# Kernel tuning notes

Hardware: AMD Instinct MI355X
Metric: run time of the kernel (lower is better)

Reference implementation:

```python
import jax, jax.numpy as jnp
import numpy as np
from jax import lax

N_SIN = 3

def _bn(x, g, b, m, v, eps):
    sh = [1] * x.ndim; sh[1] = -1
    r = lambda t: t.reshape(sh)
    return (x - r(m)) / jnp.sqrt(r(v) + eps) * r(g) + r(b)

def _conv2d(x, w, b, padding):
    y = lax.conv_general_dilated(x, w, (1, 1), padding,
                                 dimension_numbers=('NCHW', 'OIHW', 'NCHW'))
    return y + b[None, :, None, None]

def _causal_conv1d(x, w, b):
    k = w.shape[-1]
    y = lax.conv_general_dilated(x, w, (1,), [(k - 1, 0)],
                                 dimension_numbers=('NCH', 'OIH', 'NCH'))
    return y + b[None, :, None]

def _se(x, w1, w2):
    y = x.mean(axis=2)                                   # [B,C] global avg pool
    y = jax.nn.sigmoid(jax.nn.relu(y @ w1.T) @ w2.T)
    return x * y[:, :, None]

def _kan(x, W1, W2, B1, B2):
    # x: [B,din]; per-edge tiny MLP: sin/cos embed -> linear -> silu -> linear
    omega = (2.0 ** jnp.arange(N_SIN)).astype(x.dtype)   # [n_sin]
    ox = x[..., None] * omega                            # [B,din,n_sin]
    feat = jnp.concatenate([x[..., None], jnp.sin(ox), jnp.cos(ox)], axis=-1)  # [B,din,7]
    h = jnp.einsum('bif,ijhf->bijh', feat, W1) + B1[None]  # [B,din,dout,h]
    h = jax.nn.silu(h)
    out = jnp.einsum('bijh,ijh->bij', h, W2[:, :, 0, :]) + B2[None, :, :, 0]
    return out.sum(axis=1)                               # [B,dout]

def _lstm(x, w_ih, w_hh, b_ih, b_hh):
    B, T, E = x.shape
    H = w_hh.shape[1]
    def step(carry, xt):
        h, c = carry
        g = xt @ w_ih.T + h @ w_hh.T + (b_ih + b_hh)
        i, f, gg, o = jnp.split(g, 4, axis=-1)           # torch gate order i,f,g,o
        c = jax.nn.sigmoid(f) * c + jax.nn.sigmoid(i) * jnp.tanh(gg)
        h = jax.nn.sigmoid(o) * jnp.tanh(c)
        return (h, c), h
    init = (jnp.zeros((B, H), x.dtype), jnp.zeros((B, H), x.dtype))
    _, hs = lax.scan(step, init, jnp.swapaxes(x, 0, 1))
    return jnp.swapaxes(hs, 0, 1)                        # [B,T,H]

def _cluster(hidden):
    B, T, H = hidden.shape
    last = hidden[:, -1, :]
    hn = hidden / jnp.maximum(jnp.linalg.norm(hidden, axis=-1, keepdims=True), 1e-8)
    sim = jnp.einsum('bth,bsh->bts', hn, hn)
    sim = jnp.exp(-5.5 * (1.0 - sim))
    sim = sim * (1.0 - jnp.eye(T, dtype=sim.dtype))      # zero diagonal
    # 2-D prefix sums replace the O(T) python loop over block means
    S = jnp.cumsum(jnp.cumsum(sim, axis=1), axis=2)
    Sii = jnp.diagonal(S, axis1=1, axis2=2)[:, :T - 1]   # sum of [:i,:i]
    R = S[:, -1, :T - 1]                                 # sum of [:, :i]
    C = S[:, :T - 1, -1]                                 # sum of [:i, :]
    tot = S[:, -1, -1][:, None]
    i_f = jnp.arange(1, T, dtype=sim.dtype)
    dist = (Sii / i_f**2
            + (tot - R - C + Sii) / (T - i_f)**2
            - (C - Sii) / (i_f * (T - i_f))
            - (R - Sii) / (i_f * (T - i_f)))             # [B,T-1]
    cuts = jnp.argmax(dist, axis=1) + 1                  # [B]
    mask = (jnp.arange(T)[None, :] < cuts[:, None]).astype(hidden.dtype)
    corr = (hidden * mask[:, :, None]).sum(axis=1) / cuts[:, None].astype(hidden.dtype)
    return last, corr

def reference(x, we1, be1, bn_e1_g, bn_e1_b, bn_e1_m, bn_e1_v, we2, be2, bn_e2_g, bn_e2_b, bn_e2_m, bn_e2_v, w_ih, w_hh, b_ih, b_hh, mu_W1, mu_W2, mu_B1, mu_B2, std_W1, std_W2, std_B1, std_B2, muc_W1, muc_W2, muc_B1, muc_B2, stdc_W1, stdc_W2, stdc_B1, stdc_B2, fc_W1, fc_W2, fc_B1, fc_B2, wc1, bc1, bn1_g, bn1_b, bn1_m, bn1_v, se1_w1, se1_w2, wc2, bc2, bn2_g, bn2_b, bn2_m, bn2_v, se2_w1, se2_w2, wc3, bc3, bn3_g, bn3_b, bn3_m, bn3_v, eps1, eps2):
    gelu = lambda t: jax.nn.gelu(t, approximate=False)
    x = jnp.transpose(x, (0, 2, 1))                      # shuffle: [B,T,F]->[B,F,T]
    h2d = _conv2d(x[:, None], we1, be1, 'SAME')          # [B,4E,F,T]
    h2d = gelu(_bn(h2d, bn_e1_g, bn_e1_b, bn_e1_m, bn_e1_v, 1e-5))
    h2d = _conv2d(h2d, we2, be2, 'VALID')                # [B,E,1,T]
    h2d = gelu(_bn(h2d, bn_e2_g, bn_e2_b, bn_e2_m, bn_e2_v, 1e-5))
    x_src = jnp.transpose(h2d[:, :, 0, :], (0, 2, 1))    # [B,T,E]
    hseq = _lstm(x_src, w_ih, w_hh, b_ih, b_hh)          # [B,T,H]
    out, corr = _cluster(hseq)
    mu = _kan(corr, mu_W1, mu_W2, mu_B1, mu_B2)
    std = jax.nn.softplus(_kan(corr, std_W1, std_W2, std_B1, std_B2) - 5.0)
    z = mu + std * eps1
    x_z = jnp.concatenate([out, z], axis=1)              # [B,2H]
    mu_c = _kan(x_z, muc_W1, muc_W2, muc_B1, muc_B2)
    std_c = jax.nn.softplus(_kan(x_z, stdc_W1, stdc_W2, stdc_B1, stdc_B2) - 5.0)
    x1 = mu_c + std_c * eps2                             # dropout = identity (eval)
    x2 = jnp.transpose(x, (0, 2, 1))                     # [B,T,F]: channels = seq_len
    x2 = gelu(_bn(_causal_conv1d(x2, wc1, bc1), bn1_g, bn1_b, bn1_m, bn1_v, 1e-3))
    x2 = _se(x2, se1_w1, se1_w2)
    x2 = gelu(_bn(_causal_conv1d(x2, wc2, bc2), bn2_g, bn2_b, bn2_m, bn2_v, 1e-3))
    x2 = _se(x2, se2_w1, se2_w2)
    x2 = gelu(_bn(_causal_conv1d(x2, wc3, bc3), bn3_g, bn3_b, bn3_m, bn3_v, 1e-3))
    x2 = x2.mean(axis=2)                                 # [B,conv3_nf]
    x_all = jnp.concatenate([x1, x2], axis=1)            # [B, H+conv3_nf]
    return _kan(x_all, fc_W1, fc_W2, fc_B1, fc_B2)       # [B,num_classes]

def setup_inputs():
    key = jax.random.key(0)
    ks = iter(jax.random.split(key, 128))
    f32 = jnp.float32
    def n(shape, s=0.05):
        return s * jax.random.normal(next(ks), shape, f32)
    def bn_params(c):
        g = 1.0 + 0.05 * jax.random.normal(next(ks), (c,), f32)
        b = 0.05 * jax.random.normal(next(ks), (c,), f32)
        m = 0.05 * jax.random.normal(next(ks), (c,), f32)
        v = jax.random.uniform(next(ks), (c,), f32, 0.5, 1.5)
        return g, b, m, v
    def kan_params(din, dout, h=32, feat=1 + 2 * N_SIN):
        s = (2.0 / (feat + h)) ** 0.5
        return (n((din, dout, h, feat), s), n((din, dout, 1, h), s),
                jnp.zeros((din, dout, h), f32), jnp.zeros((din, dout, 1), f32))
    B, T, F_, E, H = 32, 256, 32, 64, 128
    inp = {}
    inp['x'] = jax.random.normal(next(ks), (B, T, F_), f32)
    inp['we1'] = n((4 * E, 1, 1, 8)); inp['be1'] = n((4 * E,))
    inp['bn_e1_g'], inp['bn_e1_b'], inp['bn_e1_m'], inp['bn_e1_v'] = bn_params(4 * E)
    inp['we2'] = n((E, 4 * E, F_, 1)); inp['be2'] = n((E,))
    inp['bn_e2_g'], inp['bn_e2_b'], inp['bn_e2_m'], inp['bn_e2_v'] = bn_params(E)
    inp['w_ih'] = n((4 * H, E)); inp['w_hh'] = n((4 * H, H))
    inp['b_ih'] = n((4 * H,)); inp['b_hh'] = n((4 * H,))
    for nm, (di, do) in [('mu', (H, H)), ('std', (H, H)), ('muc', (2 * H, H)), ('stdc', (2 * H, H)), ('fc', (2 * H, 10))]:
        w1, w2, b1, b2 = kan_params(di, do)
        inp[nm + '_W1'], inp[nm + '_W2'], inp[nm + '_B1'], inp[nm + '_B2'] = w1, w2, b1, b2
    inp['wc1'] = n((128, T, 8)); inp['bc1'] = n((128,))
    inp['bn1_g'], inp['bn1_b'], inp['bn1_m'], inp['bn1_v'] = bn_params(128)
    inp['se1_w1'] = n((8, 128)); inp['se1_w2'] = n((128, 8))
    inp['wc2'] = n((256, 128, 5)); inp['bc2'] = n((256,))
    inp['bn2_g'], inp['bn2_b'], inp['bn2_m'], inp['bn2_v'] = bn_params(256)
    inp['se2_w1'] = n((16, 256)); inp['se2_w2'] = n((256, 16))
    inp['wc3'] = n((128, 256, 3)); inp['bc3'] = n((128,))
    inp['bn3_g'], inp['bn3_b'], inp['bn3_m'], inp['bn3_v'] = bn_params(128)
    inp['eps1'] = jax.random.normal(next(ks), (B, H), f32)
    inp['eps2'] = jax.random.normal(next(ks), (B, H), f32)
    return inp
```

## Files before the change

### kernel.cpp

```cpp
#include <hip/hip_runtime.h>
#include <hip/hip_bf16.h>
#include <math.h>

typedef __hip_bfloat16 bf16;

#define DEV static __device__ __forceinline__

DEV float geluf(float x){ return 0.5f*x*(1.0f + erff(x*0.70710678118654752f)); }
DEV float sigmf(float x){ return 1.0f/(1.0f + __expf(-x)); }
DEV float softplusf(float x){ return (x > 15.f) ? x : log1pf(__expf(x)); }
DEV float tanhfast(float x){ float e = __expf(2.f*x); return fmaf(-2.f, 1.f/(e+1.f), 1.f); }

typedef __attribute__((ext_vector_type(8))) short v8s;
typedef __attribute__((ext_vector_type(4))) float v4f;
typedef _Float16 f16;
typedef f16 h2 __attribute__((ext_vector_type(2)));
typedef f16 f16x8 __attribute__((ext_vector_type(8)));
typedef unsigned u32x4 __attribute__((ext_vector_type(4)));

DEV float dot2f(h2 a, h2 b, float c){
#if __has_builtin(__builtin_amdgcn_fdot2)
  return __builtin_amdgcn_fdot2(a, b, c, false);
#else
  return fmaf((float)a.y, (float)b.y, fmaf((float)a.x, (float)b.x, c));
#endif
}

DEV h2 geth2(f16x8 v, int j){ h2 r; r.x = v[2*j]; r.y = v[2*j+1]; return r; }

DEV void lds_barrier(){
  asm volatile("s_waitcnt lgkmcnt(0)" ::: "memory");
  __builtin_amdgcn_s_barrier();
  __builtin_amdgcn_sched_barrier(0);
}

enum : size_t {
  OFF_W1F   = 0,
  OFF_B1F   = 2048,
  OFF_S2E   = 2304,
  OFF_B2E   = 2368,
  OFF_WIHT  = 2432,
  OFF_BIASG = 35200,
  OFF_WHHT  = 35712,
  OFF_EPI1S = 101248,
  OFF_EPI1B = 101376,
  OFF_EPI2S = 101504,
  OFF_EPI2B = 101760,
  OFF_EPI3S = 102016,
  OFF_EPI3B = 102144,
  OFF_WE2B  = 102272,
  OFF_XSRC  = 364416,
  OFF_GX    = 888704,
  OFF_HSEQ  = 5083008,
  OFF_HN    = 6131584,
  OFF_PCOL  = 7180160,
  OFF_CCOL  = 7188352,
  OFF_CUTS  = 7196544,
  OFF_LAST  = 7196576,
  OFF_CORR  = 7200672,
  OFF_FEATA = 7204768,
  OFF_XZ    = 7241632,
  OFF_FEATB = 7249824,
  OFF_WC3P  = 7315360,
  OFF_WC2P  = 7446432,
  OFF_KP    = 7708576,
  OFF_B2S   = 7741344,
  OFF_X2F   = 7839648,
  OFF_XALL  = 7843744,
  OFF_FEATC = 7851936,
  WS_FLOATS = 7909280
};

__global__ __launch_bounds__(256) void prep_kernel(
    const float* we1, const float* be1,
    const float* e1g, const float* e1b, const float* e1m, const float* e1v,
    const float* we2, const float* be2, const float* e2g, const float* e2b, const float* e2m, const float* e2v,
    const float* wih, const float* whh, const float* bih, const float* bhh,
    const float* bc1, const float* c1g, const float* c1b, const float* c1m, const float* c1v,
    const float* bc2, const float* c2g, const float* c2b, const float* c2m, const float* c2v,
    const float* bc3, const float* c3g, const float* c3b, const float* c3m, const float* c3v,
    const float* muB2, const float* sdB2, const float* mcB2, const float* scB2, const float* fcB2,
    const float* wc2, const float* wc3,
    float* ws)
{
  int idx = blockIdx.x*256 + threadIdx.x;
  if(idx < 2048){
    int o = idx>>3;
    float s = e1g[o] * rsqrtf(e1v[o] + 1e-5f);
    ws[OFF_W1F + idx] = we1[idx] * s;
  } else if(idx < 2304){
    int o = idx - 2048;
    float s = e1g[o] * rsqrtf(e1v[o] + 1e-5f);
    ws[OFF_B1F + o] = s*(be1[o] - e1m[o]) + e1b[o];
  } else if(idx < 2368){
    int e = idx - 2304;
    float s = e2g[e] * rsqrtf(e2v[e] + 1e-5f);
    ws[OFF_S2E + e] = s;
    ws[OFF_B2E + e] = s*(be2[e] - e2m[e]) + e2b[e];
  } else if(idx < 35136){
    int q = idx - 2368; int e = q>>9, g = q&511;
    ws[OFF_WIHT + q] = wih[g*64 + e];
  } else if(idx < 35648){
    int g = idx - 35136;
    ws[OFF_BIASG + g] = bih[g] + bhh[g];
  } else if(idx < 101184){
    int q = idx - 35648;
    if(q < 32768){
      int k2 = q>>9, g = q&511;
      h2 v;
      v.x = (f16)whh[g*128 + 2*k2];
      v.y = (f16)whh[g*128 + 2*k2 + 1];
      ((h2*)(ws + OFF_WHHT))[g*64 + k2] = v;
    }
  } else if(idx < 101312){
    int o = idx - 101184;
    float s = c1g[o] * rsqrtf(c1v[o] + 1e-3f);
    ws[OFF_EPI1S + o] = s;
    ws[OFF_EPI1B + o] = s*(bc1[o] - c1m[o]) + c1b[o];
  } else if(idx < 101568){
    int o = idx - 101312;
    float s = c2g[o] * rsqrtf(c2v[o] + 1e-3f);
    ws[OFF_EPI2S + o] = s;
    ws[OFF_EPI2B + o] = s*(bc2[o] - c2m[o]) + c2b[o];
  } else if(idx < 101696){
    int o = idx - 101568;
    float s = c3g[o] * rsqrtf(c3v[o] + 1e-3f);
    ws[OFF_EPI3S + o] = s;
    ws[OFF_EPI3B + o] = s*(bc3[o] - c3m[o]) + c3b[o];
  } else if(idx < 625984){
    int q = idx - 101696;
    int o = q >> 11, rem = q & 2047;
    int e = rem >> 5, f = rem & 31;
    bf16* Wr = (bf16*)(ws + OFF_WE2B);
    Wr[q] = __float2bfloat16(we2[(size_t)e*8192 + o*32 + f]);
  } else if(idx < 626112){
    int j = idx - 625984; float s = 0.f;
    for(int i=0;i<128;i++) s += muB2[i*128+j];
    ws[OFF_B2S + j] = s;
  } else if(idx < 626240){
    int j = idx - 626112; float s = 0.f;
    for(int i=0;i<128;i++) s += sdB2[i*128+j];
    ws[OFF_B2S + 128 + j] = s;
  } else if(idx < 626368){
    int j = idx - 626240; float s = 0.f;
    for(int i=0;i<256;i++) s += mcB2[i*128+j];
    ws[OFF_B2S + 256 + j] = s;
  } else if(idx < 626496){
    int j = idx - 626368; float s = 0.f;
    for(int i=0;i<256;i++) s += scB2[i*128+j];
    ws[OFF_B2S + 384 + j] = s;
  } else if(idx < 626506){
    int j = idx - 626496; float s = 0.f;
    for(int i=0;i<256;i++) s += fcB2[i*10+j];
    ws[OFF_B2S + 512 + j] = s;
  } else if(idx < 888650){
    int q = idx - 626506;
    int o = q >> 10, rem = q & 1023;
    int c = rem >> 3, k = rem & 7;
    ws[OFF_WC2P + q] = (k < 5) ? wc2[(size_t)o*640 + c*5 + k] : 0.f;
  } else if(idx < 1019722){
    int q = idx - 888650;
    int o = q >> 10, rem = q & 1023;
    int c = rem >> 2, k = rem & 3;
    ws[OFF_WC3P + q] = (k < 3) ? wc3[(size_t)o*768 + c*3 + k] : 0.f;
  }
}

__global__ __launch_bounds__(256,1) void encoder_kernel(
    const float* __restrict__ x, const float* __restrict__ w1f, const float* __restrict__ b1f,
    const float* __restrict__ s2e, const float* __restrict__ b2e,
    const bf16* __restrict__ Wr, float* __restrict__ x_src)
{
  __shared__ float xs[39*32];
  __shared__ float w1s[2048];
  __shared__ float b1s[256];
  __shared__ __align__(16) unsigned short At[2][32*136];
  __shared__ __align__(16) unsigned short Bt[2][4*2560];

  int blk = blockIdx.x; int b = blk>>3; int t0 = (blk&7)*32;
  int tid = threadIdx.x;

  for(int i=tid;i<2048;i+=256) w1s[i] = w1f[i];
  b1s[tid] = b1f[tid];
  for(int i=tid;i<39*32;i+=256){
    int r=i>>5, f=i&31; int t=t0-3+r;
    xs[i] = (t>=0 && t<256) ? x[(b*256+t)*32+f] : 0.f;
  }
  __syncthreads();

  int f = tid & 31, tq = tid >> 5;
  int lane = tid & 63, w = tid >> 6;
  int wm = w & 1, wn = w >> 1;
  int m0 = wm*16, n0 = wn*32;
  int l15 = lane & 15, quad = lane >> 4;

  const v8s* Wv = (const v8s*)Wr;

  auto stage = [&](int cc, int buf){
    v8s bw[4];
    #pragma unroll
    for(int i=0;i<4;i++) bw[i] = Wv[cc*1024 + i*256 + tid];
    unsigned short aval[16];
    #pragma unroll
    for(int ol=0;ol<4;ol++){
      int o = cc*4 + ol;
      float wv[8];
      #pragma unroll
      for(int j=0;j<8;j++) wv[j] = w1s[o*8+j];
      float bb = b1s[o];
      #pragma unroll
      for(int i=0;i<4;i++){
        int tl = tq*4 + i;
        float c = bb;
        #pragma unroll
        for(int j=0;j<8;j++) c = fmaf(wv[j], xs[(tl+j)*32+f], c);
        aval[ol*4+i] = ((__hip_bfloat16_raw)__float2bfloat16(geluf(c))).x;
      }
    }
    #pragma unroll
    for(int ol=0;ol<4;ol++){
      #pragma unroll
      for(int i=0;i<4;i++)
        At[buf][(tq*4+i)*136 + ol*32 + f] = aval[ol*4+i];
    }
    #pragma unroll
    for(int i=0;i<4;i++){
      int j = i*256 + tid;
      int ol = j>>8, e = (j&255)>>2, f8 = j&3;
      *(v8s*)&Bt[buf][ol*2560 + e*40 + f8*8] = bw[i];
    }
  };

  stage(0, 0);
  __syncthreads();

  v4f acc0 = {0.f,0.f,0.f,0.f}, acc1 = {0.f,0.f,0.f,0.f};

  for(int c=0;c<64;c++){
    int p = c & 1, q = p ^ 1;
    if(c < 63) stage(c+1, q);
    #pragma unroll
    for(int ol=0;ol<4;ol++){
      v8s av = *(const v8s*)&At[p][(m0+l15)*136 + ol*32 + quad*8];
      v8s b0 = *(const v8s*)&Bt[p][ol*2560 + (n0+l15)*40 + quad*8];
      v8s b1 = *(const v8s*)&Bt[p][ol*2560 + (n0+16+l15)*40 + quad*8];
      acc0 = __builtin_amdgcn_mfma_f32_16x16x32_bf16(av, b0, acc0, 0, 0, 0);
      acc1 = __builtin_amdgcn_mfma_f32_16x16x32_bf16(av, b1, acc1, 0, 0, 0);
    }
    __syncthreads();
  }

  #pragma unroll
  for(int r=0;r<4;r++){
    int t = t0 + m0 + quad*4 + r;
    int e0 = n0 + l15;
    float v0 = geluf(s2e[e0]*acc0[r] + b2e[e0]);
    x_src[((size_t)(b*256+t))*64 + e0] = v0;
    int e1 = e0 + 16;
    float v1 = geluf(s2e[e1]*acc1[r] + b2e[e1]);
    x_src[((size_t)(b*256+t))*64 + e1] = v1;
  }
}

__global__ __launch_bounds__(256) void gates_kernel(
    const float* x_src, const float* wihT, const float* biasg, float* gx)
{
  __shared__ float xsh[32*64];
  int blk = blockIdx.x; int b = blk>>3, t0 = (blk&7)*32;
  int tid = threadIdx.x;
  for(int i=tid;i<2048;i+=256) xsh[i] = x_src[((size_t)b*256+t0)*64 + i];
  __syncthreads();
  int g0 = tid, g1 = tid + 256;
  float acc0[32], acc1[32];
  #pragma unroll
  for(int tt=0;tt<32;tt++){ acc0[tt]=0.f; acc1[tt]=0.f; }
  for(int e=0;e<64;e++){
    float w0 = wihT[e*512+g0], w1 = wihT[e*512+g1];
    #pragma unroll
    for(int tt=0;tt<32;tt++){
      float xv = xsh[tt*64+e];
      acc0[tt] = fmaf(xv, w0, acc0[tt]);
      acc1[tt] = fmaf(xv, w1, acc1[tt]);
    }
  }
  float bg0 = biasg[g0], bg1 = biasg[g1];
  #pragma unroll
  for(int tt=0;tt<32;tt++){
    gx[((size_t)b*256+t0+tt)*512 + g0] = acc0[tt] + bg0;
    gx[((size_t)b*256+t0+tt)*512 + g1] = acc1[tt] + bg1;
  }
}

#define LSTM_STEP(GI, GF, GG, GO, PR, PW, T)                                 \
  {                                                                          \
    const f16x8* hp = (const f16x8*)&hsh[PR][half*64];                       \
    f16x8 hvv[8];                                                            \
    _Pragma("unroll")                                                        \
    for(int q=0;q<8;q++) hvv[q] = hp[q];                                     \
    float si=0.f, sf=0.f, sg=0.f, so=0.f;                                    \
    _Pragma("unroll")                                                        \
    for(int q=0;q<8;q++){                                                    \
      f16x8 Wi = __builtin_bit_cast(f16x8, wi[q]);                           \
      f16x8 Wf = __builtin_bit_cast(f16x8, wf[q]);                           \
      f16x8 Wg = __builtin_bit_cast(f16x8, wg[q]);                           \
      f16x8 Wo = __builtin_bit_cast(f16x8, wo[q]);                           \
      f16x8 hq = hvv[q];                                                     \
      _Pragma("unroll")                                                      \
      for(int j=0;j<4;j++){                                                  \
        h2 hj = geth2(hq, j);                                                \
        si = dot2f(hj, geth2(Wi,j), si);                                     \
        sf = dot2f(hj, geth2(Wf,j), sf);                                     \
        sg = dot2f(hj, geth2(Wg,j), sg);                                     \
        so = dot2f(hj, geth2(Wo,j), so);                                     \
      }                                                                      \
    }                                                                        \
    si += __shfl_xor(si, 32, 64);                                            \
    sf += __shfl_xor(sf, 32, 64);                                            \
    sg += __shfl_xor(sg, 32, 64);                                            \
    so += __shfl_xor(so, 32, 64);                                            \
    float iv = sigmf(si + (GI));                                             \
    float fv = sigmf(sf + (GF));                                             \
    float gv = tanhfast(sg + (GG));                                          \
    float ov = sigmf(so + (GO));                                             \
    c = fmaf(fv, c, iv*gv);                                                  \
    float h = ov*tanhfast(c);                                                \
    if(half == 0){                                                           \
      hsh[PW][n] = (f16)h;                                                   \
      hseq[((size_t)b*256+(T))*128 + n] = h;                                 \
    }                                                                        \
    lds_barrier();                                                           \
  }

__global__ __launch_bounds__(256)
__attribute__((amdgpu_waves_per_eu(1,1)))
void lstm_conv_kernel(
    const float* __restrict__ gates_x, const float* __restrict__ whh16f, float* __restrict__ hseq,
    const float* __restrict__ x,
    const float* __restrict__ wc1, const float* __restrict__ wc2p, const float* __restrict__ wc3p,
    const float* __restrict__ epi1s, const float* __restrict__ epi1b,
    const float* __restrict__ epi2s, const float* __restrict__ epi2b,
    const float* __restrict__ epi3s, const float* __restrict__ epi3b,
    const float* __restrict__ se1w1, const float* __restrict__ se1w2,
    const float* __restrict__ se2w1, const float* __restrict__ se2w2,
    float* __restrict__ x2f)
{
  __shared__ __align__(16) f16 hsh[2][128];
  __shared__ __align__(16) float bufA[8192];
  __shared__ __align__(16) float bufB[4096];
  __shared__ float msh[256];
  __shared__ float ysh[16];

  int tid = threadIdx.x;
  if(blockIdx.x < 32){
    int b = blockIdx.x;
    int wave = tid >> 6, lane = tid & 63;
    int half = lane >> 5;
    int n = wave*32 + (lane & 31);

    const u32x4* Wp = (const u32x4*)whh16f;
    u32x4 wi[8], wf[8], wg[8], wo[8];
    #pragma unroll
    for(int q=0;q<8;q++){
      wi[q] = Wp[(size_t)(n      )*16 + half*8 + q];
      wf[q] = Wp[(size_t)(n + 128)*16 + half*8 + q];
      wg[q] = Wp[(size_t)(n + 256)*16 + half*8 + q];
      wo[q] = Wp[(size_t)(n + 384)*16 + half*8 + q];
    }
    asm volatile("" :
      "+v"(wi[0]), "+v"(wi[1]), "+v"(wi[2]), "+v"(wi[3]),
      "+v"(wi[4]), "+v"(wi[5]), "+v"(wi[6]), "+v"(wi[7]),
      "+v"(wf[0]), "+v"(wf[1]), "+v"(wf[2]), "+v"(wf[3]),
      "+v"(wf[4]), "+v"(wf[5]), "+v"(wf[6]), "+v"(wf[7]));
    asm volatile("" :
      "+v"(wg[0]), "+v"(wg[1]), "+v"(wg[2]), "+v"(wg[3]),
      "+v"(wg[4]), "+v"(wg[5]), "+v"(wg[6]), "+v"(wg[7]),
      "+v"(wo[0]), "+v"(wo[1]), "+v"(wo[2]), "+v"(wo[3]),
      "+v"(wo[4]), "+v"(wo[5]), "+v"(wo[6]), "+v"(wo[7]));

    if(tid < 128) hsh[0][tid] = (f16)0.f;
    float c = 0.f;
    const float* gx = gates_x + (size_t)b*256*512;
    float i0v = gx[n], f0v = gx[128+n], g0v = gx[256+n], o0v = gx[384+n];
    float i1v = gx[512+n], f1v = gx[512+128+n], g1v = gx[512+256+n], o1v = gx[512+384+n];
    __syncthreads();
    for(int t=0; t<256; t+=2){
      float i2v=0.f,f2v=0.f,g2v=0.f,o2v=0.f,i3v=0.f,f3v=0.f,g3v=0.f,o3v=0.f;
      if(t+2 < 256){
        const float* gp = gx + (size_t)(t+2)*512;
        i2v = gp[n]; f2v = gp[128+n]; g2v = gp[256+n]; o2v = gp[384+n];
      }
      LSTM_STEP(i0v, f0v, g0v, o0v, 0, 1, t);
      if(t+3 < 256){
        const float* gp = gx + (size_t)(t+3)*512;
        i3v = gp[n]; f3v = gp[128+n]; g3v = gp[256+n]; o3v = gp[384+n];
      }
      LSTM_STEP(i1v, f1v, g1v, o1v, 1, 0, t+1);
      i0v=i2v; f0v=f2v; g0v=g2v; o0v=o2v;
      i1v=i3v; f1v=f3v; g1v=g3v; o1v=o3v;
    }
  } else {
    int cb = blockIdx.x - 32;
    for(int i=tid; i<8192; i+=256) bufA[i] = x[(size_t)cb*8192 + i];
    __syncthreads();

    int wv_ = tid >> 6, ln = tid & 63;
    int lh = wv_ >> 1;
    int o  = ((wv_ & 1) << 6) | ln;

    {
      float acc[16];
      #pragma unroll
      for(int j=0;j<16;j++) acc[j]=0.f;
      const float4* wp = (const float4*)(wc1 + (size_t)o*2048);
      if(lh == 0){
        for(int c=0;c<256;c++){
          const float4* rp = (const float4*)&bufA[c*32];
          float4 r0=rp[0], r1=rp[1], r2=rp[2], r3=rp[3];
          float xr[16]={r0.x,r0.y,r0.z,r0.w,r1.x,r1.y,r1.z,r1.w,
                        r2.x,r2.y,r2.z,r2.w,r3.x,r3.y,r3.z,r3.w};
          float4 w0=wp[2*c], w1=wp[2*c+1];
          float wv[8]={w0.x,w0.y,w0.z,w0.w,w1.x,w1.y,w1.z,w1.w};
          #pragma unroll
          for(int j=0;j<16;j++){
            #pragma unroll
            for(int k=0;k<8;k++){
              int idx = j + k - 7;
              if(idx >= 0) acc[j] = fmaf(xr[idx], wv[k], acc[j]);
            }
          }
        }
      } else {
        for(int c=0;c<256;c++){
          const float4* rp = (const float4*)&bufA[c*32];
          float4 r2=rp[2], r3=rp[3], r4=rp[4], r5=rp[5], r6=rp[6], r7=rp[7];
          float xr[24]={r2.x,r2.y,r2.z,r2.w,r3.x,r3.y,r3.z,r3.w,
                        r4.x,r4.y,r4.z,r4.w,r5.x,r5.y,r5.z,r5.w,
                        r6.x,r6.y,r6.z,r6.w,r7.x,r7.y,r7.z,r7.w};
          float4 w0=wp[2*c], w1=wp[2*c+1];
          float wv[8]={w0.x,w0.y,w0.z,w0.w,w1.x,w1.y,w1.z,w1.w};
          #pragma unroll
          for(int j=0;j<16;j++){
            #pragma unroll
            for(int k=0;k<8;k++)
              acc[j] = fmaf(xr[j+k+1], wv[k], acc[j]);
          }
        }
      }
      float s = epi1s[o], bb = epi1b[o];
      float g[16]; float m = 0.f;
      #pragma unroll
      for(int j=0;j<16;j++){ g[j] = geluf(s*acc[j]+bb); m += g[j]; }
      msh[lh*128 + o] = m;
      __syncthreads();
      if(tid < 8){
        float t2 = 0.f;
        for(int k=0;k<128;k++) t2 = fmaf((msh[k]+msh[128+k])*(1.f/32.f), se1w1[tid*128+k], t2);
        ysh[tid] = fmaxf(t2, 0.f);
      }
      __syncthreads();
      float t2 = 0.f;
      #pragma unroll
      for(int k=0;k<8;k++) t2 = fmaf(ysh[k], se1w2[o*8+k], t2);
      float sc = sigmf(t2);
      #pragma unroll
      for(int j=0;j<16;j++) bufB[o*32 + lh*16 + j] = g[j]*sc;
      __syncthreads();
    }

    {
      int oc = tid;
      float acc[32];
      #pragma unroll
      for(int j=0;j<32;j++) acc[j]=0.f;
      const float4* wp = (const float4*)(wc2p + (size_t)oc*1024);
      for(int c=0;c<128;c++){
        const float4* rp = (const float4*)&bufB[c*32];
        float4 r0=rp[0],r1=rp[1],r2=rp[2],r3=rp[3],r4=rp[4],r5=rp[5],r6=rp[6],r7=rp[7];
        float xr[32]={r0.x,r0.y,r0.z,r0.w,r1.x,r1.y,r1.z,r1.w,
                      r2.x,r2.y,r2.z,r2.w,r3.x,r3.y,r3.z,r3.w,
                      r4.x,r4.y,r4.z,r4.w,r5.x,r5.y,r5.z,r5.w,
                      r6.x,r6.y,r6.z,r6.w,r7.x,r7.y,r7.z,r7.w};
        float4 w0=wp[2*c], w1=wp[2*c+1];
        float wv[5]={w0.x,w0.y,w0.z,w0.w,w1.x};
        #pragma unroll
        for(int j=0;j<32;j++){
          #pragma unroll
          for(int k=0;k<5;k++){
            int idx = j + k - 4;
            if(idx >= 0) acc[j] = fmaf(xr[idx], wv[k], acc[j]);
          }
        }
      }
      float s = epi2s[oc], bb = epi2b[oc];
      float m = 0.f;
      #pragma unroll
      for(int j=0;j<32;j++){ acc[j] = geluf(s*acc[j]+bb); m += acc[j]; }
      msh[oc] = m*(1.f/32.f);
      __syncthreads();
      if(tid < 16){
        float t2 = 0.f;
        for(int k=0;k<256;k++) t2 = fmaf(msh[k], se2w1[tid*256+k], t2);
        ysh[tid] = fmaxf(t2, 0.f);
      }
      __syncthreads();
      float t2 = 0.f;
      #pragma unroll
      for(int k=0;k<16;k++) t2 = fmaf(ysh[k], se2w2[oc*16+k], t2);
      float sc = sigmf(t2);
      #pragma unroll
      for(int j=0;j<32;j++) bufA[oc*32 + j] = acc[j]*sc;
      __syncthreads();
    }

    {
      float acc[16];
      #pragma unroll
      for(int j=0;j<16;j++) acc[j]=0.f;
      const float4* wp = (const float4*)(wc3p + (size_t)o*1024);
      if(lh == 0){
        for(int c=0;c<256;c++){
          const float4* rp = (const float4*)&bufA[c*32];
          float4 r0=rp[0], r1=rp[1], r2=rp[2], r3=rp[3];
          float xr[16]={r0.x,r0.y,r0.z,r0.w,r1.x,r1.y,r1.z,r1.w,
                        r2.x,r2.y,r2.z,r2.w,r3.x,r3.y,r3.z,r3.w};
          float4 w = wp[c];
          float wv[3]={w.x,w.y,w.z};
          #pragma unroll
          for(int j=0;j<16;j++){
            #pragma unroll
            for(int k=0;k<3;k++){
              int idx = j + k - 2;
              if(idx >= 0) acc[j] = fmaf(xr[idx], wv[k], acc[j]);
            }
          }
        }
      } else {
        for(int c=0;c<256;c++){
          const float4* rp = (const float4*)&bufA[c*32];
          float4 r3=rp[3], r4=rp[4], r5=rp[5], r6=rp[6], r7=rp[7];
          float xr[20]={r3.x,r3.y,r3.z,r3.w,r4.x,r4.y,r4.z,r4.w,
                        r5.x,r5.y,r5.z,r5.w,r6.x,r6.y,r6.z,r6.w,
                        r7.x,r7.y,r7.z,r7.w};
          float4 w = wp[c];
          float wv[3]={w.x,w.y,w.z};
          #pragma unroll
          for(int j=0;j<16;j++){
            #pragma unroll
            for(int k=0;k<3;k++)
              acc[j] = fmaf(xr[j+k+2], wv[k], acc[j]);
          }
        }
      }
      float s = epi3s[o], bb = epi3b[o];
      float m = 0.f;
      #pragma unroll
      for(int j=0;j<16;j++) m += geluf(s*acc[j]+bb);
      msh[lh*128 + o] = m;
      __syncthreads();
      if(tid < 128) x2f[cb*128 + tid] = (msh[tid] + msh[128+tid])*(1.f/32.f);
    }
  }
}

__global__ __launch_bounds__(64) void hn_kernel(const float* hseq, float* hn)
{
  size_t row = blockIdx.x; int lane = threadIdx.x;
  const float* hp = hseq + row*128;
  float v0 = hp[lane], v1 = hp[lane+64];
  float ss = v0*v0 + v1*v1;
  #pragma unroll
  for(int m=1;m<64;m<<=1) ss += __shfl_xor(ss, m, 64);
  float r = 1.f / fmaxf(sqrtf(ss), 1e-8f);
  hn[row*128 + lane]      = v0*r;
  hn[row*128 + 64 + lane] = v1*r;
}

__global__ __launch_bounds__(256) void pc_kernel(const float* hn, float* pcol, float* ccol)
{
  int blk = blockIdx.x; int b = blk>>3, chunk = blk&7;
  int tid = threadIdx.x; int il = tid & 31, ts = tid >> 5;
  int i = chunk*32 + il;
  const float4* hb = (const float4*)(hn + (size_t)b*32768);
  float4 hi[32];
  #pragma unroll
  for(int r=0;r<32;r++) hi[r] = hb[(size_t)i*32 + r];
  float ps=0.f, cs=0.f;
  for(int t=ts*32; t<ts*32+32; t++){
    float dx=0.f, dy=0.f, dz=0.f, dw=0.f;
    #pragma unroll
    for(int r=0;r<32;r++){
      float4 hv = hb[(size_t)t*32 + r];
      dx = fmaf(hi[r].x, hv.x, dx);
      dy = fmaf(hi[r].y, hv.y, dy);
      dz = fmaf(hi[r].z, hv.z, dz);
      dw = fmaf(hi[r].w, hv.w, dw);
    }
    float dot = (dx+dy)+(dz+dw);
    float sim = (t==i) ? 0.f : expf(-5.5f*(1.0f - dot));
    cs += sim;
    if(t < i) ps += sim;
  }
  __shared__ float red[16][32];
  red[ts][il] = ps; red[8+ts][il] = cs;
  __syncthreads();
  if(tid < 32){
    float s=0.f;
    for(int r=0;r<8;r++) s += red[r][tid];
    pcol[b*256 + chunk*32 + tid] = s;
  } else if(tid < 64){
    int c2 = tid - 32; float s=0.f;
    for(int r=0;r<8;r++) s += red[8+r][c2];
    ccol[b*256 + chunk*32 + c2] = s;
  }
}

__global__ __launch_bounds__(256) void cutcorr_kernel(
    const float* pcol, const float* ccol, const float* hseq,
    float* last, float* corr, int* cuts)
{
  int b = blockIdx.x, tid = threadIdx.x;
  __shared__ float D[256], RC[256], dist[256];
  __shared__ int cutsh;
  if(tid == 0){
    float d=0.f, r=0.f;
    for(int i=0;i<256;i++){
      d += 2.f*pcol[b*256+i]; D[i]=d;
      r += ccol[b*256+i];     RC[i]=r;
    }
  }
  __syncthreads();
  float tot = RC[255];
  if(tid < 255){
    float Dv = D[tid], Rv = RC[tid];
    float i_f = (float)(tid+1), j_f = 256.f - i_f;
    dist[tid] = Dv/(i_f*i_f) + (tot - 2.f*Rv + Dv)/(j_f*j_f) - 2.f*(Rv - Dv)/(i_f*j_f);
  }
  __syncthreads();
  if(tid == 0){
    float best = dist[0]; int bi = 0;
    for(int i=1;i<255;i++) if(dist[i] > best){ best = dist[i]; bi = i; }
    cutsh = bi + 1; cuts[b] = cutsh;
  }
  __syncthreads();
  int cut = cutsh;
  int k = tid & 127, half = tid >> 7;
  float s = 0.f;
  for(int t=half; t<cut; t+=2) s += hseq[((size_t)b*256+t)*128 + k];
  __shared__ float partial[2][128];
  partial[half][k] = s;
  __syncthreads();
  if(tid < 128){
    corr[b*128+tid] = (partial[0][tid] + partial[1][tid]) / (float)cut;
    last[b*128+tid] = hseq[((size_t)b*256+255)*128 + tid];
  }
}

__global__ __launch_bounds__(256) void feat_kernel(const float* xin, float* feat, int n)
{
  int idx = blockIdx.x*256 + threadIdx.x;
  if(idx >= n) return;
  float xv = xin[idx];
  float* fp = feat + (size_t)idx*7;
  fp[0]=xv;
  fp[1]=sinf(xv); fp[2]=sinf(2.f*xv); fp[3]=sinf(4.f*xv);
  fp[4]=cosf(xv); fp[5]=cosf(2.f*xv); fp[6]=cosf(4.f*xv);
}

__global__ __launch_bounds__(256) void kanp2_kernel(
    const float* __restrict__ feat,
    const float* __restrict__ W1a, const float* __restrict__ B1a, const float* __restrict__ W2a,
    const float* __restrict__ W1b, const float* __restrict__ B1b, const float* __restrict__ W2b,
    int din, int dout, float* __restrict__ partial, int pstride)
{
  __shared__ float feat_s[32*225];
  __shared__ float red[8][32];
  int z = blockIdx.z;
  const float* W1 = z ? W1b : W1a;
  const float* B1 = z ? B1b : B1a;
  const float* W2 = z ? W2b : W2a;
  partial += (size_t)z * pstride;
  int j = blockIdx.x, ic = blockIdx.y;
  int i0 = ic*32;
  int tid = threadIdx.x;
  int b = tid & 31, hg = tid >> 5;
  for(int q=tid; q<1792; q+=256){
    int br = q/56, qq = q - br*56;
    float4 v = *(const float4*)(feat + ((size_t)br*din + i0)*7 + qq*4);
    float* d = &feat_s[br*225 + qq*4];
    d[0]=v.x; d[1]=v.y; d[2]=v.z; d[3]=v.w;
  }
  __syncthreads();
  float acc = 0.f;
  const float* fb = &feat_s[b*225];
  for(int ii=0; ii<32; ii++){
    int i = i0 + ii;
    size_t hbase = ((size_t)i*dout + j)*32 + hg*4;
    const float4* w1p = (const float4*)(W1 + ((size_t)i*dout + j)*224 + hg*28);
    float w1a[28];
    #pragma unroll
    for(int q=0;q<7;q++) *(float4*)&w1a[q*4] = w1p[q];
    float4 b1v = *(const float4*)(B1 + hbase);
    float4 w2v = *(const float4*)(W2 + hbase);
    float f[7];
    #pragma unroll
    for(int q=0;q<7;q++) f[q] = fb[ii*7+q];
    float b1a[4] = {b1v.x, b1v.y, b1v.z, b1v.w};
    float w2a[4] = {w2v.x, w2v.y, w2v.z, w2v.w};
    #pragma unroll
    for(int hh=0;hh<4;hh++){
      float hv = b1a[hh];
      #pragma unroll
      for(int q=0;q<7;q++) hv = fmaf(f[q], w1a[hh*7+q], hv);
      float sv = hv / (1.f + __expf(-hv));
      acc = fmaf(sv, w2a[hh], acc);
    }
  }
  red[hg][b] = acc;
  __syncthreads();
  if(tid < 32){
    float s = 0.f;
    #pragma unroll
    for(int q=0;q<8;q++) s += red[q][tid];
    partial[((size_t)ic*32 + tid)*dout + j] = s;
  }
}

__global__ __launch_bounds__(256) void kanp_kernel(
    const float* __restrict__ feat, const float* __restrict__ W1,
    const float* __restrict__ B1, const float* __restrict__ W2,
    int din, int dout, float* __restrict__ partial)
{
  __shared__ float feat_s[32*225];
  __shared__ float red[8][32];
  int j = blockIdx.x, ic = blockIdx.y;
  int i0 = ic*32;
  int tid = threadIdx.x;
  int b = tid & 31, hg = tid >> 5;
  for(int q=tid; q<1792; q+=256){
    int br = q/56, qq = q - br*56;
    float4 v = *(const float4*)(feat + ((size_t)br*din + i0)*7 + qq*4);
    float* d = &feat_s[br*225 + qq*4];
    d[0]=v.x; d[1]=v.y; d[2]=v.z; d[3]=v.w;
  }
  __syncthreads();
  float acc = 0.f;
  const float* fb = &feat_s[b*225];
  for(int ii=0; ii<32; ii++){
    int i = i0 + ii;
    size_t hbase = ((size_t)i*dout + j)*32 + hg*4;
    const float4* w1p = (const float4*)(W1 + ((size_t)i*dout + j)*224 + hg*28);
    float w1a[28];
    #pragma unroll
    for(int q=0;q<7;q++) *(float4*)&w1a[q*4] = w1p[q];
    float4 b1v = *(const float4*)(B1 + hbase);
    float4 w2v = *(const float4*)(W2 + hbase);
    float f[7];
    #pragma unroll
    for(int q=0;q<7;q++) f[q] = fb[ii*7+q];
    float b1a[4] = {b1v.x, b1v.y, b1v.z, b1v.w};
    float w2a[4] = {w2v.x, w2v.y, w2v.z, w2v.w};
    #pragma unroll
    for(int hh=0;hh<4;hh++){
      float hv = b1a[hh];
      #pragma unroll
      for(int q=0;q<7;q++) hv = fmaf(f[q], w1a[hh*7+q], hv);
      float sv = hv / (1.f + __expf(-hv));
      acc = fmaf(sv, w2a[hh], acc);
    }
  }
  red[hg][b] = acc;
  __syncthreads();
  if(tid < 32){
    float s = 0.f;
    #pragma unroll
    for(int q=0;q<8;q++) s += red[q][tid];
    partial[((size_t)ic*32 + tid)*dout + j] = s;
  }
}

__global__ __launch_bounds__(256) void kanr_kernel(
    const float* __restrict__ partial, const float* __restrict__ b2s,
    int NI, int dout, float* __restrict__ outp)
{
  int idx = blockIdx.x*256 + threadIdx.x;
  if(idx >= 32*dout) return;
  int b = idx / dout, j = idx - b*dout;
  float s = b2s[j];
  for(int ic=0; ic<NI; ic++) s += partial[((size_t)ic*32 + b)*dout + j];
  outp[idx] = s;
}

__global__ __launch_bounds__(256) void kanrz_kernel(
    const float* __restrict__ kp, const float* __restrict__ b2s,
    const float* __restrict__ eps1, const float* __restrict__ last, float* __restrict__ xz)
{
  int idx = blockIdx.x*256 + threadIdx.x;
  if(idx >= 4096) return;
  int b = idx >> 7, j = idx & 127;
  float mu = b2s[j], sd = b2s[128+j];
  #pragma unroll
  for(int ic=0; ic<4; ic++){
    mu += kp[((size_t)ic*32 + b)*128 + j];
    sd += kp[16384 + ((size_t)ic*32 + b)*128 + j];
  }
  float z = mu + softplusf(sd - 5.f)*eps1[idx];
  xz[b*256 + j]       = last[idx];
  xz[b*256 + 128 + j] = z;
}

__global__ __launch_bounds__(256) void kanrx_kernel(
    const float* __restrict__ kp, const float* __restrict__ b2s,
    const float* __restrict__ eps2, const float* __restrict__ x2f, float* __restrict__ xa)
{
  int idx = blockIdx.x*256 + threadIdx.x;
  if(idx >= 4096) return;
  int b = idx >> 7, j = idx & 127;
  float mu = b2s[256+j], sd = b2s[384+j];
  #pragma unroll
  for(int ic=0; ic<8; ic++){
    mu += kp[((size_t)ic*32 + b)*128 + j];
    sd += kp[32768 + ((size_t)ic*32 + b)*128 + j];
  }
  xa[b*256 + j]       = mu + softplusf(sd - 5.f)*eps2[idx];
  xa[b*256 + 128 + j] = x2f[idx];
}

extern "C" void kernel_launch(void* const* d_in, const int* in_sizes, int n_in,
                              void* d_out, int out_size, void* d_ws, size_t ws_size,
                              hipStream_t stream)
{
  const float* x    = (const float*)d_in[0];
  const float* we1  = (const float*)d_in[1];
  const float* be1  = (const float*)d_in[2];
  const float* e1g  = (const float*)d_in[3];
  const float* e1b  = (const float*)d_in[4];
  const float* e1m  = (const float*)d_in[5];
  const float* e1v  = (const float*)d_in[6];
  const float* we2  = (const float*)d_in[7];
  const float* be2  = (const float*)d_in[8];
  const float* e2g  = (const float*)d_in[9];
  const float* e2b  = (const float*)d_in[10];
  const float* e2m  = (const float*)d_in[11];
  const float* e2v  = (const float*)d_in[12];
  const float* wih  = (const float*)d_in[13];
  const float* whh  = (const float*)d_in[14];
  const float* bih  = (const float*)d_in[15];
  const float* bhh  = (const float*)d_in[16];
  const float* muW1 = (const float*)d_in[17];
  const float* muW2 = (const float*)d_in[18];
  const float* muB1 = (const float*)d_in[19];
  const float* muB2 = (const float*)d_in[20];
  const float* sdW1 = (const float*)d_in[21];
  const float* sdW2 = (const float*)d_in[22];
  const float* sdB1 = (const float*)d_in[23];
  const float* sdB2 = (const float*)d_in[24];
  const float* mcW1 = (const float*)d_in[25];
  const float* mcW2 = (const float*)d_in[26];
  const float* mcB1 = (const float*)d_in[27];
  const float* mcB2 = (const float*)d_in[28];
  const float* scW1 = (const float*)d_in[29];
  const float* scW2 = (const float*)d_in[30];
  const float* scB1 = (const float*)d_in[31];
  const float* scB2 = (const float*)d_in[32];
  const float* fcW1 = (const float*)d_in[33];
  const float* fcW2 = (const float*)d_in[34];
  const float* fcB1 = (const float*)d_in[35];
  const float* fcB2 = (const float*)d_in[36];
  const float* wc1  = (const float*)d_in[37];
  const float* bc1  = (const float*)d_in[38];
  const float* c1g  = (const float*)d_in[39];
  const float* c1b  = (const float*)d_in[40];
  const float* c1m  = (const float*)d_in[41];
  const float* c1v  = (const float*)d_in[42];
  const float* se1w1= (const float*)d_in[43];
  const float* se1w2= (const float*)d_in[44];
  const float* wc2  = (const float*)d_in[45];
  const float* bc2  = (const float*)d_in[46];
  const float* c2g  = (const float*)d_in[47];
  const float* c2b  = (const float*)d_in[48];
  const float* c2m  = (const float*)d_in[49];
  const float* c2v  = (const float*)d_in[50];
  const float* se2w1= (const float*)d_in[51];
  const float* se2w2= (const float*)d_in[52];
  const float* wc3  = (const float*)d_in[53];
  const float* bc3  = (const float*)d_in[54];
  const float* c3g  = (const float*)d_in[55];
  const float* c3b  = (const float*)d_in[56];
  const float* c3m  = (const float*)d_in[57];
  const float* c3v  = (const float*)d_in[58];
  const float* eps1 = (const float*)d_in[59];
  const float* eps2 = (const float*)d_in[60];

  float* ws = (float*)d_ws;
  float* kp   = ws + OFF_KP;
  float* kp2  = ws + OFF_GX;
  float* b2s  = ws + OFF_B2S;

  prep_kernel<<<3984, 256, 0, stream>>>(we1, be1, e1g,e1b,e1m,e1v,
      we2, be2,e2g,e2b,e2m,e2v, wih,whh,bih,bhh,
      bc1,c1g,c1b,c1m,c1v, bc2,c2g,c2b,c2m,c2v, bc3,c3g,c3b,c3m,c3v,
      muB2, sdB2, mcB2, scB2, fcB2, wc2, wc3, ws);

  encoder_kernel<<<256, 256, 0, stream>>>(x, ws+OFF_W1F, ws+OFF_B1F,
      ws+OFF_S2E, ws+OFF_B2E, (const bf16*)(ws+OFF_WE2B), ws+OFF_XSRC);

  gates_kernel<<<256, 256, 0, stream>>>(ws+OFF_XSRC, ws+OFF_WIHT, ws+OFF_BIASG, ws+OFF_GX);

  lstm_conv_kernel<<<64, 256, 0, stream>>>(ws+OFF_GX, ws+OFF_WHHT, ws+OFF_HSEQ,
      x, wc1, ws+OFF_WC2P, ws+OFF_WC3P,
      ws+OFF_EPI1S, ws+OFF_EPI1B, ws+OFF_EPI2S, ws+OFF_EPI2B, ws+OFF_EPI3S, ws+OFF_EPI3B,
      se1w1, se1w2, se2w1, se2w2, ws+OFF_X2F);

  hn_kernel<<<8192, 64, 0, stream>>>(ws+OFF_HSEQ, ws+OFF_HN);
  pc_kernel<<<256, 256, 0, stream>>>(ws+OFF_HN, ws+OFF_PCOL, ws+OFF_CCOL);
  cutcorr_kernel<<<32, 256, 0, stream>>>(ws+OFF_PCOL, ws+OFF_CCOL, ws+OFF_HSEQ,
      ws+OFF_LAST, ws+OFF_CORR, (int*)(ws+OFF_CUTS));

  feat_kernel<<<16, 256, 0, stream>>>(ws+OFF_CORR, ws+OFF_FEATA, 4096);
  kanp2_kernel<<<dim3(128,4,2), 256, 0, stream>>>(ws+OFF_FEATA,
      muW1, muB1, muW2, sdW1, sdB1, sdW2, 128, 128, kp, 16384);
  kanrz_kernel<<<16, 256, 0, stream>>>(kp, b2s, eps1, ws+OFF_LAST, ws+OFF_XZ);

  feat_kernel<<<32, 256, 0, stream>>>(ws+OFF_XZ, ws+OFF_FEATB, 8192);
  kanp2_kernel<<<dim3(128,8,2), 256, 0, stream>>>(ws+OFF_FEATB,
      mcW1, mcB1, mcW2, scW1, scB1, scW2, 256, 128, kp2, 32768);
  kanrx_kernel<<<16, 256, 0, stream>>>(kp2, b2s, eps2, ws+OFF_X2F, ws+OFF_XALL);

  feat_kernel<<<32, 256, 0, stream>>>(ws+OFF_XALL, ws+OFF_FEATC, 8192);
  kanp_kernel<<<dim3(10,8), 256, 0, stream>>>(ws+OFF_FEATC, fcW1, fcB1, fcW2, 256, 10, kp);
  kanr_kernel<<<2, 256, 0, stream>>>(kp, b2s+512, 8, 10, (float*)d_out);
}
```

Baseline: 866.6 us.

## Fuse normalization, feature embedding and reductions into neighboring kernels to cut launches

```diff
diff --git a/kernel.cpp b/kernel.cpp
--- a/kernel.cpp
+++ b/kernel.cpp
@@ -32,6 +32,12 @@
   asm volatile("s_waitcnt lgkmcnt(0)" ::: "memory");
   __builtin_amdgcn_s_barrier();
   __builtin_amdgcn_sched_barrier(0);
+}
+
+DEV void write_feat7(float* fp, float v){
+  fp[0]=v;
+  fp[1]=sinf(v); fp[2]=sinf(2.f*v); fp[3]=sinf(4.f*v);
+  fp[4]=cosf(v); fp[5]=cosf(2.f*v); fp[6]=cosf(4.f*v);
 }
 
 enum : size_t {
@@ -52,21 +58,17 @@
   OFF_XSRC  = 364416,
   OFF_GX    = 888704,
   OFF_HSEQ  = 5083008,
-  OFF_HN    = 6131584,
   OFF_PCOL  = 7180160,
   OFF_CCOL  = 7188352,
   OFF_CUTS  = 7196544,
   OFF_LAST  = 7196576,
-  OFF_CORR  = 7200672,
   OFF_FEATA = 7204768,
-  OFF_XZ    = 7241632,
   OFF_FEATB = 7249824,
   OFF_WC3P  = 7315360,
   OFF_WC2P  = 7446432,
   OFF_KP    = 7708576,
   OFF_B2S   = 7741344,
   OFF_X2F   = 7839648,
-  OFF_XALL  = 7843744,
   OFF_FEATC = 7851936,
   WS_FLOATS = 7909280
 };
@@ -562,28 +564,28 @@
   }
 }
 
-__global__ __launch_bounds__(64) void hn_kernel(const float* hseq, float* hn)
-{
-  size_t row = blockIdx.x; int lane = threadIdx.x;
-  const float* hp = hseq + row*128;
-  float v0 = hp[lane], v1 = hp[lane+64];
-  float ss = v0*v0 + v1*v1;
-  #pragma unroll
-  for(int m=1;m<64;m<<=1) ss += __shfl_xor(ss, m, 64);
-  float r = 1.f / fmaxf(sqrtf(ss), 1e-8f);
-  hn[row*128 + lane]      = v0*r;
-  hn[row*128 + 64 + lane] = v1*r;
-}
-
-__global__ __launch_bounds__(256) void pc_kernel(const float* hn, float* pcol, float* ccol)
+__global__ __launch_bounds__(256) void pc_kernel(const float* hseq, float* pcol, float* ccol)
 {
   int blk = blockIdx.x; int b = blk>>3, chunk = blk&7;
   int tid = threadIdx.x; int il = tid & 31, ts = tid >> 5;
   int i = chunk*32 + il;
-  const float4* hb = (const float4*)(hn + (size_t)b*32768);
+  const float4* hb = (const float4*)(hseq + (size_t)b*32768);
+  __shared__ float rnsh[256];
+  {
+    const float4* rowp = hb + (size_t)tid*32;
+    float ss = 0.f;
+    #pragma unroll
+    for(int r=0;r<32;r++){
+      float4 v = rowp[r];
+      ss = fmaf(v.x,v.x, fmaf(v.y,v.y, fmaf(v.z,v.z, fmaf(v.w,v.w, ss))));
+    }
+    rnsh[tid] = 1.f / fmaxf(sqrtf(ss), 1e-8f);
+  }
+  __syncthreads();
   float4 hi[32];
   #pragma unroll
   for(int r=0;r<32;r++) hi[r] = hb[(size_t)i*32 + r];
+  float rni = rnsh[i];
   float ps=0.f, cs=0.f;
   for(int t=ts*32; t<ts*32+32; t++){
     float dx=0.f, dy=0.f, dz=0.f, dw=0.f;
@@ -595,7 +597,7 @@
       dz = fmaf(hi[r].z, hv.z, dz);
       dw = fmaf(hi[r].w, hv.w, dw);
     }
-    float dot = (dx+dy)+(dz+dw);
+    float dot = ((dx+dy)+(dz+dw)) * rni * rnsh[t];
     float sim = (t==i) ? 0.f : expf(-5.5f*(1.0f - dot));
     cs += sim;
     if(t < i) ps += sim;
@@ -616,19 +618,23 @@
 
 __global__ __launch_bounds__(256) void cutcorr_kernel(
     const float* pcol, const float* ccol, const float* hseq,
-    float* last, float* corr, int* cuts)
+    float* last, float* featA, int* cuts)
 {
   int b = blockIdx.x, tid = threadIdx.x;
   __shared__ float D[256], RC[256], dist[256];
   __shared__ int cutsh;
-  if(tid == 0){
-    float d=0.f, r=0.f;
-    for(int i=0;i<256;i++){
-      d += 2.f*pcol[b*256+i]; D[i]=d;
-      r += ccol[b*256+i];     RC[i]=r;
-    }
-  }
-  __syncthreads();
+  D[tid]  = 2.f*pcol[b*256+tid];
+  RC[tid] = ccol[b*256+tid];
+  __syncthreads();
+  #pragma unroll
+  for(int off=1; off<256; off<<=1){
+    float dv = (tid>=off) ? D[tid-off]  : 0.f;
+    float rv = (tid>=off) ? RC[tid-off] : 0.f;
+    __syncthreads();
+    D[tid]  += dv;
+    RC[tid] += rv;
+    __syncthreads();
+  }
   float tot = RC[255];
   if(tid < 255){
     float Dv = D[tid], Rv = RC[tid];
@@ -650,20 +656,10 @@
   partial[half][k] = s;
   __syncthreads();
   if(tid < 128){
-    corr[b*128+tid] = (partial[0][tid] + partial[1][tid]) / (float)cut;
+    float cv = (partial[0][tid] + partial[1][tid]) / (float)cut;
     last[b*128+tid] = hseq[((size_t)b*256+255)*128 + tid];
-  }
-}
-
-__global__ __launch_bounds__(256) void feat_kernel(const float* xin, float* feat, int n)
-{
-  int idx = blockIdx.x*256 + threadIdx.x;
-  if(idx >= n) return;
-  float xv = xin[idx];
-  float* fp = feat + (size_t)idx*7;
-  fp[0]=xv;
-  fp[1]=sinf(xv); fp[2]=sinf(2.f*xv); fp[3]=sinf(4.f*xv);
-  fp[4]=cosf(xv); fp[5]=cosf(2.f*xv); fp[6]=cosf(4.f*xv);
+    write_feat7(featA + ((size_t)(b*128+tid))*7, cv);
+  }
 }
 
 __global__ __launch_bounds__(256) void kanp2_kernel(
@@ -725,74 +721,9 @@
   }
 }
 
-__global__ __launch_bounds__(256) void kanp_kernel(
-    const float* __restrict__ feat, const float* __restrict__ W1,
-    const float* __restrict__ B1, const float* __restrict__ W2,
-    int din, int dout, float* __restrict__ partial)
-{
-  __shared__ float feat_s[32*225];
-  __shared__ float red[8][32];
-  int j = blockIdx.x, ic = blockIdx.y;
-  int i0 = ic*32;
-  int tid = threadIdx.x;
-  int b = tid & 31, hg = tid >> 5;
-  for(int q=tid; q<1792; q+=256){
-    int br = q/56, qq = q - br*56;
-    float4 v = *(const float4*)(feat + ((size_t)br*din + i0)*7 + qq*4);
-    float* d = &feat_s[br*225 + qq*4];
-    d[0]=v.x; d[1]=v.y; d[2]=v.z; d[3]=v.w;
-  }
-  __syncthreads();
-  float acc = 0.f;
-  const float* fb = &feat_s[b*225];
-  for(int ii=0; ii<32; ii++){
-    int i = i0 + ii;
-    size_t hbase = ((size_t)i*dout + j)*32 + hg*4;
-    const float4* w1p = (const float4*)(W1 + ((size_t)i*dout + j)*224 + hg*28);
-    float w1a[28];
-    #pragma unroll
-    for(int q=0;q<7;q++) *(float4*)&w1a[q*4] = w1p[q];
-    float4 b1v = *(const float4*)(B1 + hbase);
-    float4 w2v = *(const float4*)(W2 + hbase);
-    float f[7];
-    #pragma unroll
-    for(int q=0;q<7;q++) f[q] = fb[ii*7+q];
-    float b1a[4] = {b1v.x, b1v.y, b1v.z, b1v.w};
-    float w2a[4] = {w2v.x, w2v.y, w2v.z, w2v.w};
-    #pragma unroll
-    for(int hh=0;hh<4;hh++){
-      float hv = b1a[hh];
-      #pragma unroll
-      for(int q=0;q<7;q++) hv = fmaf(f[q], w1a[hh*7+q], hv);
-      float sv = hv / (1.f + __expf(-hv));
-      acc = fmaf(sv, w2a[hh], acc);
-    }
-  }
-  red[hg][b] = acc;
-  __syncthreads();
-  if(tid < 32){
-    float s = 0.f;
-    #pragma unroll
-    for(int q=0;q<8;q++) s += red[q][tid];
-    partial[((size_t)ic*32 + tid)*dout + j] = s;
-  }
-}
-
-__global__ __launch_bounds__(256) void kanr_kernel(
-    const float* __restrict__ partial, const float* __restrict__ b2s,
-    int NI, int dout, float* __restrict__ outp)
-{
-  int idx = blockIdx.x*256 + threadIdx.x;
-  if(idx >= 32*dout) return;
-  int b = idx / dout, j = idx - b*dout;
-  float s = b2s[j];
-  for(int ic=0; ic<NI; ic++) s += partial[((size_t)ic*32 + b)*dout + j];
-  outp[idx] = s;
-}
-
 __global__ __launch_bounds__(256) void kanrz_kernel(
     const float* __restrict__ kp, const float* __restrict__ b2s,
-    const float* __restrict__ eps1, const float* __restrict__ last, float* __restrict__ xz)
+    const float* __restrict__ eps1, const float* __restrict__ last, float* __restrict__ featB)
 {
   int idx = blockIdx.x*256 + threadIdx.x;
   if(idx >= 4096) return;
@@ -804,13 +735,14 @@
     sd += kp[16384 + ((size_t)ic*32 + b)*128 + j];
   }
   float z = mu + softplusf(sd - 5.f)*eps1[idx];
-  xz[b*256 + j]       = last[idx];
-  xz[b*256 + 128 + j] = z;
+  float lv = last[idx];
+  write_feat7(featB + ((size_t)(b*256 + j))*7, lv);
+  write_feat7(featB + ((size_t)(b*256 + 128 + j))*7, z);
 }
 
 __global__ __launch_bounds__(256) void kanrx_kernel(
     const float* __restrict__ kp, const float* __restrict__ b2s,
-    const float* __restrict__ eps2, const float* __restrict__ x2f, float* __restrict__ xa)
+    const float* __restrict__ eps2, const float* __restrict__ x2f, float* __restrict__ featC)
 {
   int idx = blockIdx.x*256 + threadIdx.x;
   if(idx >= 4096) return;
@@ -821,8 +753,66 @@
     mu += kp[((size_t)ic*32 + b)*128 + j];
     sd += kp[32768 + ((size_t)ic*32 + b)*128 + j];
   }
-  xa[b*256 + j]       = mu + softplusf(sd - 5.f)*eps2[idx];
-  xa[b*256 + 128 + j] = x2f[idx];
+  float v0 = mu + softplusf(sd - 5.f)*eps2[idx];
+  float v1 = x2f[idx];
+  write_feat7(featC + ((size_t)(b*256 + j))*7, v0);
+  write_feat7(featC + ((size_t)(b*256 + 128 + j))*7, v1);
+}
+
+__global__ __launch_bounds__(256) void kanpfc_kernel(
+    const float* __restrict__ feat, const float* __restrict__ W1,
+    const float* __restrict__ B1, const float* __restrict__ W2,
+    const float* __restrict__ b2s_fc, float* __restrict__ outp)
+{
+  __shared__ float feat_s[32*225];
+  __shared__ float red[8][32];
+  int j = blockIdx.x;
+  int tid = threadIdx.x;
+  int b = tid & 31, hg = tid >> 5;
+  float acc = 0.f;
+  for(int ic=0; ic<8; ic++){
+    int i0 = ic*32;
+    __syncthreads();
+    for(int q=tid; q<1792; q+=256){
+      int br = q/56, qq = q - br*56;
+      float4 v = *(const float4*)(feat + ((size_t)br*256 + i0)*7 + qq*4);
+      float* d = &feat_s[br*225 + qq*4];
+      d[0]=v.x; d[1]=v.y; d[2]=v.z; d[3]=v.w;
+    }
+    __syncthreads();
+    const float* fb = &feat_s[b*225];
+    for(int ii=0; ii<32; ii++){
+      int i = i0 + ii;
+      size_t hbase = ((size_t)i*10 + j)*32 + hg*4;
+      const float4* w1p = (const float4*)(W1 + ((size_t)i*10 + j)*224 + hg*28);
+      float w1a[28];
+      #pragma unroll
+      for(int q=0;q<7;q++) *(float4*)&w1a[q*4] = w1p[q];
+      float4 b1v = *(const float4*)(B1 + hbase);
+      float4 w2v = *(const float4*)(W2 + hbase);
+      float f[7];
+      #pragma unroll
+      for(int q=0;q<7;q++) f[q] = fb[ii*7+q];
+      float b1a[4] = {b1v.x, b1v.y, b1v.z, b1v.w};
+      float w2a[4] = {w2v.x, w2v.y, w2v.z, w2v.w};
+      #pragma unroll
+      for(int hh=0;hh<4;hh++){
+        float hv = b1a[hh];
+        #pragma unroll
+        for(int q=0;q<7;q++) hv = fmaf(f[q], w1a[hh*7+q], hv);
+        float sv = hv / (1.f + __expf(-hv));
+        acc = fmaf(sv, w2a[hh], acc);
+      }
+    }
+  }
+  red[hg][b] = acc;
+  __syncthreads();
+  if(tid < 32){
+    float s = b2s_fc[j];
+    #pragma unroll
+    for(int q=0;q<8;q++) s += red[q][tid];
+    outp[tid*10 + j] = s;
+  }
 }
 
 extern "C" void kernel_launch(void* const* d_in, const int* in_sizes, int n_in,
@@ -911,22 +901,18 @@
       ws+OFF_EPI1S, ws+OFF_EPI1B, ws+OFF_EPI2S, ws+OFF_EPI2B, ws+OFF_EPI3S, ws+OFF_EPI3B,
       se1w1, se1w2, se2w1, se2w2, ws+OFF_X2F);
 
-  hn_kernel<<<8192, 64, 0, stream>>>(ws+OFF_HSEQ, ws+OFF_HN);
-  pc_kernel<<<256, 256, 0, stream>>>(ws+OFF_HN, ws+OFF_PCOL, ws+OFF_CCOL);
+  pc_kernel<<<256, 256, 0, stream>>>(ws+OFF_HSEQ, ws+OFF_PCOL, ws+OFF_CCOL);
   cutcorr_kernel<<<32, 256, 0, stream>>>(ws+OFF_PCOL, ws+OFF_CCOL, ws+OFF_HSEQ,
-      ws+OFF_LAST, ws+OFF_CORR, (int*)(ws+OFF_CUTS));
-
-  feat_kernel<<<16, 256, 0, stream>>>(ws+OFF_CORR, ws+OFF_FEATA, 4096);
+      ws+OFF_LAST, ws+OFF_FEATA, (int*)(ws+OFF_CUTS));
+
   kanp2_kernel<<<dim3(128,4,2), 256, 0, stream>>>(ws+OFF_FEATA,
       muW1, muB1, muW2, sdW1, sdB1, sdW2, 128, 128, kp, 16384);
-  kanrz_kernel<<<16, 256, 0, stream>>>(kp, b2s, eps1, ws+OFF_LAST, ws+OFF_XZ);
-
-  feat_kernel<<<32, 256, 0, stream>>>(ws+OFF_XZ, ws+OFF_FEATB, 8192);
+  kanrz_kernel<<<16, 256, 0, stream>>>(kp, b2s, eps1, ws+OFF_LAST, ws+OFF_FEATB);
+
   kanp2_kernel<<<dim3(128,8,2), 256, 0, stream>>>(ws+OFF_FEATB,
       mcW1, mcB1, mcW2, scW1, scB1, scW2, 256, 128, kp2, 32768);
-  kanrx_kernel<<<16, 256, 0, stream>>>(kp2, b2s, eps2, ws+OFF_X2F, ws+OFF_XALL);
-
-  feat_kernel<<<32, 256, 0, stream>>>(ws+OFF_XALL, ws+OFF_FEATC, 8192);
-  kanp_kernel<<<dim3(10,8), 256, 0, stream>>>(ws+OFF_FEATC, fcW1, fcB1, fcW2, 256, 10, kp);
-  kanr_kernel<<<2, 256, 0, stream>>>(kp, b2s+512, 8, 10, (float*)d_out);
-}
+  kanrx_kernel<<<16, 256, 0, stream>>>(kp2, b2s, eps2, ws+OFF_X2F, ws+OFF_FEATC);
+
+  kanpfc_kernel<<<10, 256, 0, stream>>>(ws+OFF_FEATC, fcW1, fcB1, fcW2,
+      b2s+512, (float*)d_out);
+}
```

After: 1.025 ms. 1.18x slower.
